# Kernel optimization log

Measured on AMD Instinct MI355X. Metric: run time of the kernel, lower is better.

Reference implementation:

```python
import jax, jax.numpy as jnp
import numpy as np

N, E, R, D = 100000, 600000, 3, 128  # nodes, edges per relation, relations, hidden


def setup_inputs() -> dict:
    key = jax.random.key(0)
    ks = jax.random.split(key, 12)
    sc = 1.0 / np.sqrt(D)
    return dict(
        x=jax.random.normal(ks[0], (N, D), jnp.float32),
        edge_src=jax.random.randint(ks[1], (R, E), 0, N, jnp.int32),
        edge_dst=jax.random.randint(ks[2], (R, E), 0, N, jnp.int32),
        edge_w=jax.random.uniform(ks[3], (R, E), jnp.float32),
        W=jax.random.normal(ks[4], (R, D, D), jnp.float32) * sc,
        attn_l=jax.random.normal(ks[5], (R, D), jnp.float32) * sc,
        attn_r=jax.random.normal(ks[6], (R, D), jnp.float32) * sc,
        gat_b=jnp.zeros((R, D), jnp.float32),
        bi_w=jax.random.normal(ks[7], (D, D), jnp.float32) * sc,
        bi_b=jnp.zeros((D,), jnp.float32),
        si_w=jax.random.normal(ks[8], (D, D), jnp.float32) * sc,
        si_b=jnp.zeros((D,), jnp.float32),
        res_w=jax.random.normal(ks[9], (), jnp.float32),
        ln_g=jnp.ones((D,), jnp.float32),
        ln_b=jnp.zeros((D,), jnp.float32),
    )


def _leaky(x, slope):
    return jnp.where(x >= 0, x, slope * x)


def _gat(x, W, al, ar, b, src, dst, ew):
    # DGL GATConv, 1 head, edge-weighted: h = xW; e = LReLU(a_l.h_src + a_r.h_dst);
    # alpha = edge_softmax(e per dst) * edge_weight; out[d] = sum alpha * h_src + bias.
    h = x @ W                                   # (N, D)
    el = (h * al).sum(-1)                       # (N,)
    er = (h * ar).sum(-1)                       # (N,)
    e = _leaky(el[src] + er[dst], 0.2)          # (E,)
    m = jax.ops.segment_max(e, dst, num_segments=N)
    a = jnp.exp(e - m[dst])
    s = jax.ops.segment_sum(a, dst, num_segments=N)
    alpha = a / s[dst] * ew                     # (E,)
    out = jax.ops.segment_sum(alpha[:, None] * h[src], dst, num_segments=N)
    return out + b                              # zero-indegree nodes -> bias only


def reference(x, edge_src, edge_dst, edge_w, W, attn_l, attn_r, gat_b,
              bi_w, bi_b, si_w, si_b, res_w, ln_g, ln_b):
    # per-relation intra aggregation, stacked along relation axis: (N, R, D)
    feats = jnp.stack(
        [_gat(x, W[r], attn_l[r], attn_r[r], gat_b[r],
              edge_src[r], edge_dst[r], edge_w[r]) for r in range(R)], axis=1)
    # FM-style bi-interaction over the relation axis
    s = feats.sum(axis=1)                       # (N, D)
    deep_fm = 0.5 * (s ** 2 - (feats ** 2).sum(axis=1))
    nfm = _leaky(deep_fm @ bi_w.T + bi_b, 0.01) + _leaky(s @ si_w.T + si_b, 0.01)
    # gated residual + LayerNorm
    out = nfm + x * jax.nn.sigmoid(res_w)
    mu = out.mean(-1, keepdims=True)
    var = ((out - mu) ** 2).mean(-1, keepdims=True)
    return (out - mu) * jax.lax.rsqrt(var + 1e-5) * ln_g + ln_b
```

## Files before the change

kernel.cpp:

```cpp
#include <hip/hip_runtime.h>

#define DD 128
typedef unsigned int u32;
typedef __attribute__((ext_vector_type(8))) short bf16x8;
typedef __attribute__((ext_vector_type(4))) float f32x4;

__device__ __forceinline__ float lrelu(float v, float s) { return v >= 0.f ? v : s * v; }
__device__ __forceinline__ ushort f2bf(float f) {
  union { float f; u32 u; } v; v.f = f;
  u32 u = v.u;
  return (ushort)((u + 0x7FFFu + ((u >> 16) & 1u)) >> 16);
}

union frag_cvt { uint4 u; bf16x8 h; };

__global__ __launch_bounds__(256) void k_prep_w(const float* __restrict__ W,
                                                short* __restrict__ WA)
{
  int t = blockIdx.x * 256 + threadIdx.x;
  int lane = t & 63, ks = (t >> 6) & 3, cf = (t >> 8) & 7, r = t >> 11;
  int c = cf * 16 + (lane & 15);
  int kb = ks * 32 + (lane >> 4) * 8;
  const float* Wr = W + (size_t)r * DD * DD;
  ushort o[8];
#pragma unroll
  for (int j = 0; j < 8; j++) o[j] = f2bf(Wr[(size_t)(kb + j) * DD + c]);
  uint4 st;
  st.x = (u32)o[0] | ((u32)o[1] << 16);
  st.y = (u32)o[2] | ((u32)o[3] << 16);
  st.z = (u32)o[4] | ((u32)o[5] << 16);
  st.w = (u32)o[6] | ((u32)o[7] << 16);
  *(uint4*)(WA + (size_t)t * 8) = st;
}

__global__ __launch_bounds__(256) void k_prep_cw(const float* __restrict__ bw,
                                                 const float* __restrict__ sw,
                                                 short* __restrict__ WB)
{
  int t = blockIdx.x * 256 + threadIdx.x;
  int lane = t & 63, ks = (t >> 6) & 3, cf = (t >> 8) & 7, m = t >> 11;
  const float* src = m ? sw : bw;
  int c = cf * 16 + (lane & 15);
  int k = ks * 32 + (lane >> 4) * 8;
  const float* pr = src + (size_t)c * DD + k;
  uint4 st;
  st.x = (u32)f2bf(pr[0]) | ((u32)f2bf(pr[1]) << 16);
  st.y = (u32)f2bf(pr[2]) | ((u32)f2bf(pr[3]) << 16);
  st.z = (u32)f2bf(pr[4]) | ((u32)f2bf(pr[5]) << 16);
  st.w = (u32)f2bf(pr[6]) | ((u32)f2bf(pr[7]) << 16);
  *(uint4*)(WB + (size_t)t * 8) = st;
}

__global__ void k_prep_av(const float* __restrict__ W, const float* __restrict__ al,
                          const float* __restrict__ ar, float* __restrict__ wl,
                          float* __restrict__ wr)
{
  int t = blockIdx.x * 192 + threadIdx.x;
  if (t >= 384) return;
  int r = t >> 7, k = t & 127;
  const float* Wrow = W + (size_t)r * DD * DD + (size_t)k * DD;
  const float* alr = al + r * DD;
  const float* arr = ar + r * DD;
  float pl = 0.f, pr = 0.f;
  for (int c = 0; c < DD; c++) { float w = Wrow[c]; pl = fmaf(w, alr[c], pl); pr = fmaf(w, arr[c], pr); }
  wl[t] = pl; wr[t] = pr;
}

__global__ __launch_bounds__(256) void k_prep_xrow(
    const float* __restrict__ x, const float* __restrict__ wl, const float* __restrict__ wr,
    u32* __restrict__ xrow, float* __restrict__ el, float* __restrict__ er, int N)
{
  const int wid = (int)(((long long)blockIdx.x * 256 + threadIdx.x) >> 6);
  const int lane = threadIdx.x & 63;
  if (wid >= N) return;
  float2 xv = *(const float2*)(x + (size_t)wid * DD + lane * 2);
  xrow[(size_t)wid * 64 + lane] = (u32)f2bf(xv.x) | ((u32)f2bf(xv.y) << 16);
  float d[6];
#pragma unroll
  for (int r = 0; r < 3; r++) {
    float2 wlv = *(const float2*)(wl + r * DD + lane * 2);
    float2 wrv = *(const float2*)(wr + r * DD + lane * 2);
    d[r]     = xv.x * wlv.x + xv.y * wlv.y;
    d[r + 3] = xv.x * wrv.x + xv.y * wrv.y;
  }
#pragma unroll
  for (int o = 32; o; o >>= 1) {
#pragma unroll
    for (int k = 0; k < 6; k++) d[k] += __shfl_xor(d[k], o);
  }
  if (lane == 0) {
#pragma unroll
    for (int r = 0; r < 3; r++) {
      el[(size_t)r * N + wid] = d[r];
      er[(size_t)r * N + wid] = d[r + 3];
    }
  }
}

__global__ void k_hist3(const int* __restrict__ dst, int* __restrict__ cnt, int N, int E) {
  int i = blockIdx.x * 256 + threadIdx.x;
  int r = blockIdx.y;
  if (i < E) atomicAdd(cnt + (size_t)r * N + dst[(size_t)r * E + i], 1);
}

__global__ __launch_bounds__(256) void k_scan_bsum(const int* __restrict__ cnt,
                                                   int* __restrict__ bsum, int M)
{
  __shared__ int red[256];
  const int t = threadIdx.x;
  const int g0 = blockIdx.x * 2048 + t * 8;
  int s = 0;
#pragma unroll
  for (int j = 0; j < 8; j++) { int i = g0 + j; if (i < M) s += cnt[i]; }
  red[t] = s;
  __syncthreads();
  for (int o = 128; o; o >>= 1) {
    if (t < o) red[t] += red[t + o];
    __syncthreads();
  }
  if (t == 0) bsum[blockIdx.x] = red[0];
}

__global__ __launch_bounds__(256) void k_scan_btop(const int* __restrict__ bsum,
                                                   int* __restrict__ bpre, int NB)
{
  __shared__ int sums[256];
  const int t = threadIdx.x;
  int v = (t < NB) ? bsum[t] : 0;
  sums[t] = v;
  __syncthreads();
  for (int o = 1; o < 256; o <<= 1) {
    int u = (t >= o) ? sums[t - o] : 0;
    __syncthreads();
    sums[t] += u;
    __syncthreads();
  }
  if (t < NB) bpre[t] = sums[t] - v;
}

__global__ __launch_bounds__(256) void k_scan_base(const int* __restrict__ cnt,
    const int* __restrict__ bpre, int* __restrict__ base, int M)
{
  __shared__ int sums[256];
  const int t = threadIdx.x;
  const int g0 = blockIdx.x * 2048 + t * 8;
  int c[8];
  int ts = 0;
#pragma unroll
  for (int j = 0; j < 8; j++) { int i = g0 + j; c[j] = (i < M) ? cnt[i] : 0; ts += c[j]; }
  sums[t] = ts;
  __syncthreads();
  for (int o = 1; o < 256; o <<= 1) {
    int u = (t >= o) ? sums[t - o] : 0;
    __syncthreads();
    sums[t] += u;
    __syncthreads();
  }
  int run = bpre[blockIdx.x] + sums[t] - ts;
#pragma unroll
  for (int j = 0; j < 8; j++) {
    int i = g0 + j;
    if (i <= M) base[i] = run;
    run += c[j];
  }
}

__global__ void k_scatter3(const int* __restrict__ src, const int* __restrict__ dst,
    const float* __restrict__ ew, const float* __restrict__ el, const float* __restrict__ er,
    const int* __restrict__ base, int* __restrict__ cnt, int4* __restrict__ meta,
    int N, int E)
{
  int i = blockIdx.x * 256 + threadIdx.x;
  if (i >= E) return;
  int r = blockIdx.y;
  size_t ei = (size_t)r * E + i;
  int d = dst[ei], s = src[ei];
  size_t node = (size_t)r * N + d;
  int pos = base[node] + (atomicSub(cnt + node, 1) - 1);
  float e = lrelu(el[(size_t)r * N + s] + er[node], 0.2f);
  meta[pos] = make_int4(s, __float_as_int(e), __float_as_int(ew[ei]), 0);
}

__global__ __launch_bounds__(256) void k_node_agg3(
    const int* __restrict__ base, const int4* __restrict__ meta,
    const u32* __restrict__ xrow, u32* __restrict__ aggx, int N, int Np)
{
  const int wid = (int)(((long long)blockIdx.x * 256 + threadIdx.x) >> 6);
  const int lane = threadIdx.x & 63;
  if (wid >= N) return;
  const char* xb = (const char*)xrow;
  const u32 lb = (u32)lane << 2;

  int b0[3], dg[3];
#pragma unroll
  for (int r = 0; r < 3; r++) {
    int v0 = base[r * N + wid];
    int v1 = base[r * N + wid + 1];
    b0[r] = v0; dg[r] = v1 - v0;
  }

  float A0[3] = {0.f, 0.f, 0.f}, A1[3] = {0.f, 0.f, 0.f}, SS[3];

  if (dg[0] <= 64 && dg[1] <= 64 && dg[2] <= 64) {
    int sv[3]; float av[3], cwv[3];
#pragma unroll
    for (int r = 0; r < 3; r++) {
      int s = 0; float a = 0.f, c = 0.f;
      if (lane < dg[r]) {
        int4 mm = meta[b0[r] + lane];
        s = mm.x;
        a = __expf(fminf(__int_as_float(mm.y), 60.f));
        c = a * __int_as_float(mm.z);
      }
      sv[r] = s; av[r] = a; cwv[r] = c;
    }
#pragma unroll
    for (int r = 0; r < 3; r++) {
      float s = av[r];
#pragma unroll
      for (int o = 32; o; o >>= 1) s += __shfl_xor(s, o);
      SS[r] = s;
    }
    float cc[3][8]; u32 oo[3][8];
#pragma unroll
    for (int r = 0; r < 3; r++)
#pragma unroll
      for (int q = 0; q < 8; q++) {
        cc[r][q] = __shfl(cwv[r], q);
        oo[r][q] = ((u32)__shfl(sv[r], q) << 8) | lb;
      }
    u32 uu[3][8];
#pragma unroll
    for (int r = 0; r < 3; r++)
#pragma unroll
      for (int q = 0; q < 8; q++) uu[r][q] = *(const u32*)(xb + oo[r][q]);
#pragma unroll
    for (int r = 0; r < 3; r++)
#pragma unroll
      for (int q = 0; q < 8; q++) {
        A0[r] = fmaf(cc[r][q], __uint_as_float(uu[r][q] << 16), A0[r]);
        A1[r] = fmaf(cc[r][q], __uint_as_float(uu[r][q] & 0xFFFF0000u), A1[r]);
      }
#pragma unroll
    for (int r = 0; r < 3; r++) {
      for (int c8 = 8; c8 < dg[r]; c8 += 8) {
        float c2[8]; u32 o2[8];
#pragma unroll
        for (int q = 0; q < 8; q++) {
          c2[q] = __shfl(cwv[r], c8 + q);
          o2[q] = ((u32)__shfl(sv[r], c8 + q) << 8) | lb;
        }
        u32 u2[8];
#pragma unroll
        for (int q = 0; q < 8; q++) u2[q] = *(const u32*)(xb + o2[q]);
#pragma unroll
        for (int q = 0; q < 8; q++) {
          A0[r] = fmaf(c2[q], __uint_as_float(u2[q] << 16), A0[r]);
          A1[r] = fmaf(c2[q], __uint_as_float(u2[q] & 0xFFFF0000u), A1[r]);
        }
      }
    }
  } else {
#pragma unroll
    for (int r = 0; r < 3; r++) {
      float sp = 0.f;
      for (int c0 = 0; c0 < dg[r]; c0 += 64) {
        int kk = min(64, dg[r] - c0);
        int s = 0; float a = 0.f, c = 0.f;
        if (lane < kk) {
          int4 mm = meta[b0[r] + c0 + lane];
          s = mm.x;
          a = __expf(fminf(__int_as_float(mm.y), 60.f));
          c = a * __int_as_float(mm.z);
        }
        sp += a;
        for (int c8 = 0; c8 < kk; c8 += 8) {
          float c2[8]; u32 o2[8];
#pragma unroll
          for (int q = 0; q < 8; q++) {
            c2[q] = __shfl(c, c8 + q);
            o2[q] = ((u32)__shfl(s, c8 + q) << 8) | lb;
          }
          u32 u2[8];
#pragma unroll
          for (int q = 0; q < 8; q++) u2[q] = *(const u32*)(xb + o2[q]);
#pragma unroll
          for (int q = 0; q < 8; q++) {
            A0[r] = fmaf(c2[q], __uint_as_float(u2[q] << 16), A0[r]);
            A1[r] = fmaf(c2[q], __uint_as_float(u2[q] & 0xFFFF0000u), A1[r]);
          }
        }
      }
#pragma unroll
      for (int o = 32; o; o >>= 1) sp += __shfl_xor(sp, o);
      SS[r] = sp;
    }
  }

#pragma unroll
  for (int r = 0; r < 3; r++) {
    const float inv = (dg[r] > 0) ? 1.f / SS[r] : 0.f;
    aggx[((size_t)r * Np + wid) * 64 + lane] =
        (u32)f2bf(A0[r] * inv) | ((u32)f2bf(A1[r] * inv) << 16);
  }
}

__global__ __launch_bounds__(512) void k_feats(
    const u32* __restrict__ aggx, const short* __restrict__ WA,
    const float* __restrict__ gb, u32* __restrict__ sfrag, u32* __restrict__ dfrag,
    int Np, int ntiles)
{
  extern __shared__ u32 ldsf[];
  u32* lwa = ldsf;
  const int tid = threadIdx.x;
  const int lane = tid & 63;
  const int w = tid >> 6;
  u32* wbuf = ldsf + 24576 + w * 1088;

  for (int i = tid; i < 6144; i += 512)
    *(uint4*)&lwa[i * 4] = *(const uint4*)(WA + (size_t)i * 8);
  __syncthreads();

  const int nl = lane & 15, fh = lane >> 4;

  for (int tile = blockIdx.x; tile < ntiles; tile += gridDim.x) {
    const int tb = tile * 128 + w * 16;
    const int nblk = tile * 8 + w;
    f32x4 sa[8], qa[8];
#pragma unroll
    for (int cf = 0; cf < 8; cf++) { sa[cf] = (f32x4){0,0,0,0}; qa[cf] = (f32x4){0,0,0,0}; }

    for (int r = 0; r < 3; r++) {
#pragma unroll
      for (int rr = 0; rr < 16; rr++)
        wbuf[rr * 68 + lane] = aggx[((size_t)r * Np + tb + rr) * 64 + lane];
      bf16x8 bf[4];
#pragma unroll
      for (int ks = 0; ks < 4; ks++) {
        frag_cvt cv;
        cv.u = *(const uint4*)&wbuf[nl * 68 + ks * 16 + fh * 4];
        bf[ks] = cv.h;
      }
      f32x4 acc[8];
#pragma unroll
      for (int cf = 0; cf < 8; cf++) acc[cf] = (f32x4){0,0,0,0};
#pragma unroll
      for (int ks = 0; ks < 4; ks++) {
#pragma unroll
        for (int cf = 0; cf < 8; cf++) {
          frag_cvt av;
          av.u = *(const uint4*)&lwa[(((r * 8 + cf) * 4 + ks) * 64 + lane) * 4];
          acc[cf] = __builtin_amdgcn_mfma_f32_16x16x32_bf16(av.h, bf[ks], acc[cf], 0, 0, 0);
        }
      }
#pragma unroll
      for (int cf = 0; cf < 8; cf++) {
        float4 g4 = *(const float4*)(gb + r * DD + cf * 16 + fh * 4);
        const float* gp = (const float*)&g4;
#pragma unroll
        for (int j = 0; j < 4; j++) {
          float f = acc[cf][j] + gp[j];
          sa[cf][j] += f;
          qa[cf][j] += f * f;
        }
      }
    }

#pragma unroll
    for (int cf = 0; cf < 8; cf++) {
      int wb = cf * 8 + fh * 2;
      wbuf[nl * 68 + wb]     = (u32)f2bf(sa[cf][0]) | ((u32)f2bf(sa[cf][1]) << 16);
      wbuf[nl * 68 + wb + 1] = (u32)f2bf(sa[cf][2]) | ((u32)f2bf(sa[cf][3]) << 16);
    }
#pragma unroll
    for (int ks = 0; ks < 4; ks++) {
      uint4 v = *(const uint4*)&wbuf[nl * 68 + ks * 16 + fh * 4];
      *(uint4*)&sfrag[(((size_t)nblk * 4 + ks) * 64 + lane) * 4] = v;
    }
#pragma unroll
    for (int cf = 0; cf < 8; cf++) {
      int wb = cf * 8 + fh * 2;
      float d0 = 0.5f * (sa[cf][0] * sa[cf][0] - qa[cf][0]);
      float d1 = 0.5f * (sa[cf][1] * sa[cf][1] - qa[cf][1]);
      float d2 = 0.5f * (sa[cf][2] * sa[cf][2] - qa[cf][2]);
      float d3 = 0.5f * (sa[cf][3] * sa[cf][3] - qa[cf][3]);
      wbuf[nl * 68 + wb]     = (u32)f2bf(d0) | ((u32)f2bf(d1) << 16);
      wbuf[nl * 68 + wb + 1] = (u32)f2bf(d2) | ((u32)f2bf(d3) << 16);
    }
#pragma unroll
    for (int ks = 0; ks < 4; ks++) {
      uint4 v = *(const uint4*)&wbuf[nl * 68 + ks * 16 + fh * 4];
      *(uint4*)&dfrag[(((size_t)nblk * 4 + ks) * 64 + lane) * 4] = v;
    }
  }
}

__global__ __launch_bounds__(512) void k_comb(
    const u32* __restrict__ sfrag, const u32* __restrict__ dfrag,
    const float* __restrict__ x, const short* __restrict__ WB,
    const float* __restrict__ bi_b, const float* __restrict__ si_b,
    const float* __restrict__ res_w, const float* __restrict__ ln_g,
    const float* __restrict__ ln_b, float* __restrict__ out, int N, int ntiles)
{
  extern __shared__ u32 ldsc[];
  u32* lwb = ldsc;
  const int tid = threadIdx.x;
  const int lane = tid & 63;
  const int w = tid >> 6;
  float* obuf = (float*)(ldsc + 16384) + w * 2112;

  for (int i = tid; i < 4096; i += 512)
    *(uint4*)&lwb[i * 4] = *(const uint4*)(WB + (size_t)i * 8);
  __syncthreads();

  const int nl = lane & 15, fh = lane >> 4;
  const float sigw = 1.f / (1.f + __expf(-res_w[0]));
  const float2 g2 = *(const float2*)(ln_g + lane * 2);
  const float2 b2 = *(const float2*)(ln_b + lane * 2);

  for (int tile = blockIdx.x; tile < ntiles; tile += gridDim.x) {
    const int tb = tile * 128 + w * 16;
    const int nblk = tile * 8 + w;
    const int node = tb + nl;

    bf16x8 sf[4], df[4];
#pragma unroll
    for (int ks = 0; ks < 4; ks++) {
      frag_cvt cs, cd;
      cs.u = *(const uint4*)&sfrag[(((size_t)nblk * 4 + ks) * 64 + lane) * 4];
      cd.u = *(const uint4*)&dfrag[(((size_t)nblk * 4 + ks) * 64 + lane) * 4];
      sf[ks] = cs.h; df[ks] = cd.h;
    }
    f32x4 accB[8], accS[8];
#pragma unroll
    for (int cf = 0; cf < 8; cf++) {
      accB[cf] = (f32x4){0,0,0,0};
      accS[cf] = (f32x4){0,0,0,0};
    }
#pragma unroll
    for (int ks = 0; ks < 4; ks++) {
#pragma unroll
      for (int cf = 0; cf < 8; cf++) {
        frag_cvt ab, as;
        ab.u = *(const uint4*)&lwb[(((0 * 8 + cf) * 4 + ks) * 64 + lane) * 4];
        as.u = *(const uint4*)&lwb[(((1 * 8 + cf) * 4 + ks) * 64 + lane) * 4];
        accB[cf] = __builtin_amdgcn_mfma_f32_16x16x32_bf16(ab.h, df[ks], accB[cf], 0, 0, 0);
        accS[cf] = __builtin_amdgcn_mfma_f32_16x16x32_bf16(as.h, sf[ks], accS[cf], 0, 0, 0);
      }
    }

    float sv = 0.f, sq = 0.f;
#pragma unroll
    for (int cf = 0; cf < 8; cf++) {
      int c0 = cf * 16 + fh * 4;
      float4 bb4 = *(const float4*)(bi_b + c0);
      float4 sb4 = *(const float4*)(si_b + c0);
      float4 xv = make_float4(0.f, 0.f, 0.f, 0.f);
      if (node < N) xv = *(const float4*)(x + (size_t)node * DD + c0);
      const float* bbp = (const float*)&bb4;
      const float* sbp = (const float*)&sb4;
      const float* xvp = (const float*)&xv;
      float4 o;
      float* op = (float*)&o;
#pragma unroll
      for (int j = 0; j < 4; j++) {
        float val = lrelu(accB[cf][j] + bbp[j], 0.01f)
                  + lrelu(accS[cf][j] + sbp[j], 0.01f)
                  + xvp[j] * sigw;
        op[j] = val;
        sv += val; sq += val * val;
      }
      *(float4*)&obuf[nl * 132 + c0] = o;
    }
    sv += __shfl_xor(sv, 16); sq += __shfl_xor(sq, 16);
    sv += __shfl_xor(sv, 32); sq += __shfl_xor(sq, 32);
    const float mu = sv * (1.f / DD);
    const float var = sq * (1.f / DD) - mu * mu;
    const float rs = rsqrtf(var + 1e-5f);

#pragma unroll
    for (int rr = 0; rr < 16; rr++) {
      int n2 = tb + rr;
      if (n2 >= N) continue;
      float mur = __shfl(mu, rr);
      float rsr = __shfl(rs, rr);
      float2 v = *(const float2*)&obuf[rr * 132 + lane * 2];
      float2 o;
      o.x = (v.x - mur) * rsr * g2.x + b2.x;
      o.y = (v.y - mur) * rsr * g2.y + b2.y;
      *(float2*)(out + (size_t)n2 * DD + lane * 2) = o;
    }
  }
}

extern "C" void kernel_launch(void* const* d_in, const int* in_sizes, int n_in,
                              void* d_out, int out_size, void* d_ws, size_t ws_size,
                              hipStream_t stream)
{
  const float* x    = (const float*)d_in[0];
  const int*   esrc = (const int*)d_in[1];
  const int*   edst = (const int*)d_in[2];
  const float* ew   = (const float*)d_in[3];
  const float* W    = (const float*)d_in[4];
  const float* al   = (const float*)d_in[5];
  const float* ar   = (const float*)d_in[6];
  const float* gb   = (const float*)d_in[7];
  const float* bi_w = (const float*)d_in[8];
  const float* bi_b = (const float*)d_in[9];
  const float* si_w = (const float*)d_in[10];
  const float* si_b = (const float*)d_in[11];
  const float* res_w= (const float*)d_in[12];
  const float* ln_g = (const float*)d_in[13];
  const float* ln_b = (const float*)d_in[14];

  const int N = in_sizes[0] / DD;
  const int R = 3;
  const int E = in_sizes[1] / R;
  const int Np = ((N + 127) / 128) * 128;
  const int M = R * N;
  const int NB = (M + 2047) / 2048;
  const int ntiles = Np / 128;

  auto al256 = [](size_t v) { return (v + 255) & ~(size_t)255; };
  char* p = (char*)d_ws;
  u32*   xrow  = (u32*)p;
  u32*   sfrag = (u32*)p;
  p += al256((size_t)Np * 64 * 4);
  u32*   aggx  = (u32*)p;  p += al256((size_t)R * Np * 64 * 4);
  int4*  meta  = (int4*)p;
  u32*   dfrag = (u32*)p;
  p += al256((size_t)R * E * 16);
  float* el    = (float*)p; p += al256((size_t)M * 4);
  float* er    = (float*)p; p += al256((size_t)M * 4);
  int*   cnt   = (int*)p;   p += al256((size_t)M * 4);
  int*   base  = (int*)p;   p += al256(((size_t)M + 1) * 4);
  short* WA    = (short*)p; p += al256((size_t)R * 8 * 4 * 64 * 8 * 2);
  short* WB    = (short*)p; p += al256((size_t)2 * 8 * 4 * 64 * 8 * 2);
  float* wl    = (float*)p; p += al256((size_t)R * DD * 4);
  float* wr    = (float*)p; p += al256((size_t)R * DD * 4);
  int*   bsum  = (int*)p;   p += 1024;
  int*   bpre  = (int*)p;   p += 1024;

  const int egrid = (E + 255) / 256;
  const int DYN_LDS = 133120;

  hipFuncSetAttribute((const void*)k_feats,
                      hipFuncAttributeMaxDynamicSharedMemorySize, DYN_LDS);
  hipFuncSetAttribute((const void*)k_comb,
                      hipFuncAttributeMaxDynamicSharedMemorySize, DYN_LDS);

  k_prep_w<<<24, 256, 0, stream>>>(W, WA);
  k_prep_cw<<<16, 256, 0, stream>>>(bi_w, si_w, WB);
  k_prep_av<<<2, 192, 0, stream>>>(W, al, ar, wl, wr);
  k_prep_xrow<<<(N + 3) / 4, 256, 0, stream>>>(x, wl, wr, xrow, el, er, N);

  hipMemsetAsync(cnt, 0, (size_t)M * 4, stream);
  k_hist3<<<dim3(egrid, 3), 256, 0, stream>>>(edst, cnt, N, E);
  k_scan_bsum<<<NB, 256, 0, stream>>>(cnt, bsum, M);
  k_scan_btop<<<1, 256, 0, stream>>>(bsum, bpre, NB);
  k_scan_base<<<NB, 256, 0, stream>>>(cnt, bpre, base, M);
  k_scatter3<<<dim3(egrid, 3), 256, 0, stream>>>(esrc, edst, ew, el, er,
                                                 base, cnt, meta, N, E);
  k_node_agg3<<<(N + 3) / 4, 256, 0, stream>>>(base, meta, xrow, aggx, N, Np);
  k_feats<<<256, 512, DYN_LDS, stream>>>(aggx, WA, gb, sfrag, dfrag, Np, ntiles);
  k_comb<<<256, 512, DYN_LDS, stream>>>(sfrag, dfrag, x, WB, bi_b, si_b,
                                        res_w, ln_g, ln_b, (float*)d_out, N, ntiles);
}
```

Before: 394.8 us.

## Record histogram ranks to drop scatter atomics and pack base with er

The histogram kernel now saves each edge's atomic return value as its rank within its destination bucket. The scatter then computes its position as base plus rank, with no second atomicSub pass over the counts. The per-node CSR base and er value are packed into one int2, so the scatter fetches both with a single random load. In exchange, the histogram writes an extra rank array, which aliases the aggx buffer, and node_agg3 reads base at a stride of 8 bytes instead of 4.

```diff
diff --git a/kernel.cpp b/kernel.cpp
--- a/kernel.cpp
+++ b/kernel.cpp
@@ -68,7 +68,7 @@
 
 __global__ __launch_bounds__(256) void k_prep_xrow(
     const float* __restrict__ x, const float* __restrict__ wl, const float* __restrict__ wr,
-    u32* __restrict__ xrow, float* __restrict__ el, float* __restrict__ er, int N)
+    u32* __restrict__ xrow, float* __restrict__ el, int2* __restrict__ bex, int N)
 {
   const int wid = (int)(((long long)blockIdx.x * 256 + threadIdx.x) >> 6);
   const int lane = threadIdx.x & 63;
@@ -92,15 +92,19 @@
 #pragma unroll
     for (int r = 0; r < 3; r++) {
       el[(size_t)r * N + wid] = d[r];
-      er[(size_t)r * N + wid] = d[r + 3];
-    }
-  }
-}
-
-__global__ void k_hist3(const int* __restrict__ dst, int* __restrict__ cnt, int N, int E) {
+      bex[(size_t)r * N + wid].y = __float_as_int(d[r + 3]);
+    }
+  }
+}
+
+__global__ void k_hist3(const int* __restrict__ dst, int* __restrict__ cnt,
+                        int* __restrict__ rank, int N, int E) {
   int i = blockIdx.x * 256 + threadIdx.x;
   int r = blockIdx.y;
-  if (i < E) atomicAdd(cnt + (size_t)r * N + dst[(size_t)r * E + i], 1);
+  if (i < E) {
+    size_t ei = (size_t)r * E + i;
+    rank[ei] = atomicAdd(cnt + (size_t)r * N + dst[ei], 1);
+  }
 }
 
 __global__ __launch_bounds__(256) void k_scan_bsum(const int* __restrict__ cnt,
@@ -139,7 +143,7 @@
 }
 
 __global__ __launch_bounds__(256) void k_scan_base(const int* __restrict__ cnt,
-    const int* __restrict__ bpre, int* __restrict__ base, int M)
+    const int* __restrict__ bpre, int2* __restrict__ bex, int M)
 {
   __shared__ int sums[256];
   const int t = threadIdx.x;
@@ -160,29 +164,29 @@
 #pragma unroll
   for (int j = 0; j < 8; j++) {
     int i = g0 + j;
-    if (i <= M) base[i] = run;
+    if (i <= M) bex[i].x = run;
     run += c[j];
   }
 }
 
 __global__ void k_scatter3(const int* __restrict__ src, const int* __restrict__ dst,
-    const float* __restrict__ ew, const float* __restrict__ el, const float* __restrict__ er,
-    const int* __restrict__ base, int* __restrict__ cnt, int4* __restrict__ meta,
-    int N, int E)
+    const float* __restrict__ ew, const float* __restrict__ el,
+    const int* __restrict__ rank, const int2* __restrict__ bex,
+    int4* __restrict__ meta, int N, int E)
 {
   int i = blockIdx.x * 256 + threadIdx.x;
   if (i >= E) return;
   int r = blockIdx.y;
   size_t ei = (size_t)r * E + i;
   int d = dst[ei], s = src[ei];
-  size_t node = (size_t)r * N + d;
-  int pos = base[node] + (atomicSub(cnt + node, 1) - 1);
-  float e = lrelu(el[(size_t)r * N + s] + er[node], 0.2f);
+  int2 be = bex[(size_t)r * N + d];
+  int pos = be.x + rank[ei];
+  float e = lrelu(el[(size_t)r * N + s] + __int_as_float(be.y), 0.2f);
   meta[pos] = make_int4(s, __float_as_int(e), __float_as_int(ew[ei]), 0);
 }
 
 __global__ __launch_bounds__(256) void k_node_agg3(
-    const int* __restrict__ base, const int4* __restrict__ meta,
+    const int2* __restrict__ bex, const int4* __restrict__ meta,
     const u32* __restrict__ xrow, u32* __restrict__ aggx, int N, int Np)
 {
   const int wid = (int)(((long long)blockIdx.x * 256 + threadIdx.x) >> 6);
@@ -194,8 +198,8 @@
   int b0[3], dg[3];
 #pragma unroll
   for (int r = 0; r < 3; r++) {
-    int v0 = base[r * N + wid];
-    int v1 = base[r * N + wid + 1];
+    int v0 = bex[r * N + wid].x;
+    int v1 = bex[r * N + wid + 1].x;
     b0[r] = v0; dg[r] = v1 - v0;
   }
 
@@ -526,14 +530,15 @@
   u32*   xrow  = (u32*)p;
   u32*   sfrag = (u32*)p;
   p += al256((size_t)Np * 64 * 4);
-  u32*   aggx  = (u32*)p;  p += al256((size_t)R * Np * 64 * 4);
+  int*   rank  = (int*)p;
+  u32*   aggx  = (u32*)p;
+  p += al256((size_t)R * Np * 64 * 4);
   int4*  meta  = (int4*)p;
   u32*   dfrag = (u32*)p;
   p += al256((size_t)R * E * 16);
   float* el    = (float*)p; p += al256((size_t)M * 4);
-  float* er    = (float*)p; p += al256((size_t)M * 4);
+  int2*  bex   = (int2*)p;  p += al256(((size_t)M + 1) * 8);
   int*   cnt   = (int*)p;   p += al256((size_t)M * 4);
-  int*   base  = (int*)p;   p += al256(((size_t)M + 1) * 4);
   short* WA    = (short*)p; p += al256((size_t)R * 8 * 4 * 64 * 8 * 2);
   short* WB    = (short*)p; p += al256((size_t)2 * 8 * 4 * 64 * 8 * 2);
   float* wl    = (float*)p; p += al256((size_t)R * DD * 4);
@@ -552,16 +557,16 @@
   k_prep_w<<<24, 256, 0, stream>>>(W, WA);
   k_prep_cw<<<16, 256, 0, stream>>>(bi_w, si_w, WB);
   k_prep_av<<<2, 192, 0, stream>>>(W, al, ar, wl, wr);
-  k_prep_xrow<<<(N + 3) / 4, 256, 0, stream>>>(x, wl, wr, xrow, el, er, N);
+  k_prep_xrow<<<(N + 3) / 4, 256, 0, stream>>>(x, wl, wr, xrow, el, bex, N);
 
   hipMemsetAsync(cnt, 0, (size_t)M * 4, stream);
-  k_hist3<<<dim3(egrid, 3), 256, 0, stream>>>(edst, cnt, N, E);
+  k_hist3<<<dim3(egrid, 3), 256, 0, stream>>>(edst, cnt, rank, N, E);
   k_scan_bsum<<<NB, 256, 0, stream>>>(cnt, bsum, M);
   k_scan_btop<<<1, 256, 0, stream>>>(bsum, bpre, NB);
-  k_scan_base<<<NB, 256, 0, stream>>>(cnt, bpre, base, M);
-  k_scatter3<<<dim3(egrid, 3), 256, 0, stream>>>(esrc, edst, ew, el, er,
-                                                 base, cnt, meta, N, E);
-  k_node_agg3<<<(N + 3) / 4, 256, 0, stream>>>(base, meta, xrow, aggx, N, Np);
+  k_scan_base<<<NB, 256, 0, stream>>>(cnt, bpre, bex, M);
+  k_scatter3<<<dim3(egrid, 3), 256, 0, stream>>>(esrc, edst, ew, el, rank, bex,
+                                                 meta, N, E);
+  k_node_agg3<<<(N + 3) / 4, 256, 0, stream>>>(bex, meta, xrow, aggx, N, Np);
   k_feats<<<256, 512, DYN_LDS, stream>>>(aggx, WA, gb, sfrag, dfrag, Np, ntiles);
   k_comb<<<256, 512, DYN_LDS, stream>>>(sfrag, dfrag, x, WB, bi_b, si_b,
                                         res_w, ln_g, ln_b, (float*)d_out, N, ntiles);
```

After: 366.6 us. 7.1% less time.
